# Kernel tuning notes

Hardware: AMD Instinct MI355X
Metric: run time of the kernel (lower is better)

The kernel has to match this reference:

```python
import jax, jax.numpy as jnp
import numpy as np

B, TIN, TOUT = 128, 512, 64
IN_F, OUT_F, H = 64, 32, 1024
DEC_IN = IN_F + OUT_F  # decoder GRU input size


def setup_inputs() -> dict:
    key = jax.random.key(0)
    ks = jax.random.split(key, 24)
    s = 1.0 / np.sqrt(H)
    u = lambda k, shp: jax.random.uniform(k, shp, jnp.float32, -s, s)
    return {
        "enc_input": jax.random.normal(ks[0], (B, TIN, IN_F), jnp.float32),
        "dec_input": jax.random.normal(ks[1], (B, TOUT, IN_F), jnp.float32),
        # encoder GRU, layer 0 (input IN_F) and layer 1 (input H); gates stacked [r,z,n]
        "enc_Wih0": u(ks[2], (3 * H, IN_F)), "enc_Whh0": u(ks[3], (3 * H, H)),
        "enc_bih0": u(ks[4], (3 * H,)), "enc_bhh0": u(ks[5], (3 * H,)),
        "enc_Wih1": u(ks[6], (3 * H, H)), "enc_Whh1": u(ks[7], (3 * H, H)),
        "enc_bih1": u(ks[8], (3 * H,)), "enc_bhh1": u(ks[9], (3 * H,)),
        # decoder GRU, layer 0 (input DEC_IN) and layer 1 (input H)
        "dec_Wih0": u(ks[10], (3 * H, DEC_IN)), "dec_Whh0": u(ks[11], (3 * H, H)),
        "dec_bih0": u(ks[12], (3 * H,)), "dec_bhh0": u(ks[13], (3 * H,)),
        "dec_Wih1": u(ks[14], (3 * H, H)), "dec_Whh1": u(ks[15], (3 * H, H)),
        "dec_bih1": u(ks[16], (3 * H,)), "dec_bhh1": u(ks[17], (3 * H,)),
        # output MLP: Linear(H,H)+ReLU, then Linear(H,OUT_F, bias=False)
        "out1_W": u(ks[18], (H, H)), "out1_b": u(ks[19], (H,)),
        "out2_W": u(ks[20], (OUT_F, H)),
    }


def _gru_cell(x, h, Wih, Whh, bih, bhh):
    """Single GRU step, PyTorch gate convention. x:(B,in) h:(B,H) -> (B,H)."""
    gi = x @ Wih.T + bih
    gh = h @ Whh.T + bhh
    ir, iz, inn = jnp.split(gi, 3, axis=-1)
    hr, hz, hn = jnp.split(gh, 3, axis=-1)
    r = jax.nn.sigmoid(ir + hr)
    z = jax.nn.sigmoid(iz + hz)
    n = jnp.tanh(inn + r * hn)
    return (1.0 - z) * n + z * h


def _gru_layer(x, h0, Wih, Whh, bih, bhh):
    """Full-sequence GRU layer. x:(B,T,in) -> (ys:(B,T,H), hT:(B,H))."""
    xp = jnp.einsum('bti,gi->btg', x, Wih) + bih  # precompute input projections
    def step(h, g):
        gh = h @ Whh.T + bhh
        ir, iz, inn = jnp.split(g, 3, axis=-1)
        hr, hz, hn = jnp.split(gh, 3, axis=-1)
        r = jax.nn.sigmoid(ir + hr)
        z = jax.nn.sigmoid(iz + hz)
        n = jnp.tanh(inn + r * hn)
        hnew = (1.0 - z) * n + z * h
        return hnew, hnew
    hT, ys = jax.lax.scan(step, h0, jnp.swapaxes(xp, 0, 1))
    return jnp.swapaxes(ys, 0, 1), hT


def _forward(enc_input, dec_input,
             enc_Wih0, enc_Whh0, enc_bih0, enc_bhh0,
             enc_Wih1, enc_Whh1, enc_bih1, enc_bhh1,
             dec_Wih0, dec_Whh0, dec_bih0, dec_bhh0,
             dec_Wih1, dec_Whh1, dec_bih1, dec_bhh1,
             out1_W, out1_b, out2_W):
    b = enc_input.shape[0]
    zeros = jnp.zeros((b, H), enc_input.dtype)
    # encoder: 2-layer GRU from zero state
    y0, eh0 = _gru_layer(enc_input, zeros, enc_Wih0, enc_Whh0, enc_bih0, enc_bhh0)
    _, eh1 = _gru_layer(y0, zeros, enc_Wih1, enc_Whh1, enc_bih1, enc_bhh1)
    y_prev0 = enc_input[:, -1, :OUT_F]
    def dec_step(carry, x_t):
        y_prev, h0, h1 = carry
        x = jnp.concatenate([y_prev, x_t], axis=-1)  # (B, OUT_F+IN_F)
        h0n = _gru_cell(x, h0, dec_Wih0, dec_Whh0, dec_bih0, dec_bhh0)
        h1n = _gru_cell(h0n, h1, dec_Wih1, dec_Whh1, dec_bih1, dec_bhh1)
        out = jax.nn.relu(h1n @ out1_W.T + out1_b) @ out2_W.T  # dropout=identity (eval)
        return (out, h0n, h1n), out
    _, ys = jax.lax.scan(dec_step, (y_prev0, eh0, eh1), jnp.swapaxes(dec_input, 0, 1))
    return jnp.swapaxes(ys, 0, 1)  # (B, TOUT, OUT_F)


def reference(enc_input, dec_input,
              enc_Wih0, enc_Whh0, enc_bih0, enc_bhh0,
              enc_Wih1, enc_Whh1, enc_bih1, enc_bhh1,
              dec_Wih0, dec_Whh0, dec_bih0, dec_bhh0,
              dec_Wih1, dec_Whh1, dec_bih1, dec_bhh1,
              out1_W, out1_b, out2_W):
    return _forward(enc_input, dec_input,
                    enc_Wih0, enc_Whh0, enc_bih0, enc_bhh0,
                    enc_Wih1, enc_Whh1, enc_bih1, enc_bhh1,
                    dec_Wih0, dec_Whh0, dec_bih0, dec_bhh0,
                    dec_Wih1, dec_Whh1, dec_bih1, dec_bhh1,
                    out1_W, out1_b, out2_W)
```

## Files before the change

### kernel.cpp

```cpp
#include <hip/hip_runtime.h>

typedef unsigned short u16;
typedef unsigned long long u64;
typedef __attribute__((ext_vector_type(8))) short bf16x8;
typedef __attribute__((ext_vector_type(4))) float f32x4;

#define Bsz   128
#define TIN   512
#define TOUT  64
#define INF   64
#define OUTF  32
#define Hdim  1024
#define H3    3072

#define K0    1088
#define K1    2048
#define KD0   1120
#define KD1   2048
#define KH    1024

#define SX0  (Bsz * K0)
#define SX1  (Bsz * K1)
#define SXD0 (Bsz * KD0)
#define SXD1 (Bsz * KD1)
#define SH   (Bsz * Hdim)

#define BAR_ROOT 512
#define BAR_GEN  528
#define BAR_WORDS 544

__device__ __forceinline__ u16 f2bf(float f) {
    union { float f; unsigned u; } c; c.f = f;
    unsigned u = c.u;
    unsigned r = (u + 0x7fffu + ((u >> 16) & 1u)) >> 16;
    return (u16)r;
}

__device__ __forceinline__ f32x4 mfma16(bf16x8 a, bf16x8 b, f32x4 c) {
    return __builtin_amdgcn_mfma_f32_16x16x32_bf16(a, b, c, 0, 0, 0);
}

__device__ __forceinline__ void tile_map32(int wg, int& htile, int& bq) {
    const int xcd = wg & 7, idx = wg >> 3;
    htile = ((idx & 3) << 3) + xcd;
    bq = idx >> 2;
}

__device__ __forceinline__ u64 ald64(const void* p) {
    return __hip_atomic_load((const u64*)p, __ATOMIC_RELAXED, __HIP_MEMORY_SCOPE_AGENT);
}
__device__ __forceinline__ void ast64(void* p, u64 v) {
    __hip_atomic_store((u64*)p, v, __ATOMIC_RELAXED, __HIP_MEMORY_SCOPE_AGENT);
}
__device__ __forceinline__ float aldf(const float* p) {
    return __hip_atomic_load(p, __ATOMIC_RELAXED, __HIP_MEMORY_SCOPE_AGENT);
}
__device__ __forceinline__ void astf(float* p, float v) {
    __hip_atomic_store(p, v, __ATOMIC_RELAXED, __HIP_MEMORY_SCOPE_AGENT);
}
__device__ __forceinline__ u16 aldu16(const u16* p) {
    return __hip_atomic_load(p, __ATOMIC_RELAXED, __HIP_MEMORY_SCOPE_AGENT);
}
__device__ __forceinline__ void astu16(u16* p, u16 v) {
    __hip_atomic_store(p, v, __ATOMIC_RELAXED, __HIP_MEMORY_SCOPE_AGENT);
}
__device__ __forceinline__ bf16x8 ldx(const u16* p) {
    union { u64 q[2]; bf16x8 v; } u;
    u.q[0] = ald64(p);
    u.q[1] = ald64(p + 4);
    return u.v;
}

__device__ __forceinline__ void gridbar(unsigned* bar, unsigned target) {
    __syncthreads();
    if (threadIdx.x == 0) {
        asm volatile("s_waitcnt vmcnt(0) lgkmcnt(0)" ::: "memory");
        unsigned leaf = (blockIdx.x >> 3) << 4;
        unsigned a = __hip_atomic_fetch_add(&bar[leaf], 1u,
                        __ATOMIC_RELAXED, __HIP_MEMORY_SCOPE_AGENT);
        if (((a + 1u) & 7u) == 0u) {
            unsigned r = __hip_atomic_fetch_add(&bar[BAR_ROOT], 1u,
                            __ATOMIC_RELAXED, __HIP_MEMORY_SCOPE_AGENT);
            if (((r + 1u) & 31u) == 0u)
                __hip_atomic_fetch_add(&bar[BAR_GEN], 1u,
                        __ATOMIC_RELAXED, __HIP_MEMORY_SCOPE_AGENT);
        }
        while (__hip_atomic_load(&bar[BAR_GEN],
                    __ATOMIC_RELAXED, __HIP_MEMORY_SCOPE_AGENT) < target)
            __builtin_amdgcn_s_sleep(2);
        asm volatile("" ::: "memory");
    }
    __syncthreads();
}

template <int K>
__device__ __forceinline__ void stage_x(const u16* __restrict__ Xsrc, u16* __restrict__ xl) {
    const int tid = threadIdx.x;
    const int r = tid >> 4, tj = tid & 15;
    const u16* srow = Xsrc + (size_t)r * K;
    const unsigned base = (unsigned)(r * K * 2);
    const unsigned swz = (unsigned)((r & 7) << 4);
    constexpr int U = K / 4;
    for (int k0 = tj; k0 < U; k0 += 128) {
        u64 tmp[8];
#pragma unroll
        for (int i = 0; i < 8; ++i) {
            int k4 = k0 + i * 16;
            if (k4 < U) tmp[i] = ald64(srow + k4 * 4);
        }
#pragma unroll
        for (int i = 0; i < 8; ++i) {
            int k4 = k0 + i * 16;
            if (k4 < U) *(u64*)((char*)xl + ((base + (unsigned)k4 * 8u) ^ swz)) = tmp[i];
        }
    }
}

template <int KB0, int KB1, int SPLIT, int K>
__device__ __forceinline__ void gru_wave_lds(
        const u16* __restrict__ W, const u16* __restrict__ xl,
        int j0w, int row,
        f32x4& accR, f32x4& accZ, f32x4& accN0, f32x4& accN1) {
    const int lane = threadIdx.x & 63;
    const int l15 = lane & 15, kq = lane >> 4;
    const u16* Wr = W + (size_t)(j0w + l15) * K + kq * 8;
    const u16* Wz = Wr + (size_t)1024 * K;
    const u16* Wn = Wz + (size_t)1024 * K;
    const unsigned xbase = (unsigned)(row * K * 2 + kq * 16);
    const unsigned swz = (unsigned)((row & 7) << 4);
    accR = (f32x4){0.f, 0.f, 0.f, 0.f};
    accZ = (f32x4){0.f, 0.f, 0.f, 0.f};
    accN0 = (f32x4){0.f, 0.f, 0.f, 0.f};
    accN1 = (f32x4){0.f, 0.f, 0.f, 0.f};
    constexpr int E0 = (SPLIT < KB1) ? SPLIT : KB1;
    constexpr int S1 = (SPLIT > KB0) ? SPLIT : KB0;
#pragma unroll 8
    for (int kb = KB0; kb < E0; ++kb) {
        const int o = kb * 32;
        bf16x8 xb = *(const bf16x8*)((const char*)xl + ((xbase + (unsigned)kb * 64u) ^ swz));
        accR  = mfma16(*(const bf16x8*)(Wr + o), xb, accR);
        accZ  = mfma16(*(const bf16x8*)(Wz + o), xb, accZ);
        accN0 = mfma16(*(const bf16x8*)(Wn + o), xb, accN0);
    }
#pragma unroll 8
    for (int kb = S1; kb < KB1; ++kb) {
        const int o = kb * 32;
        bf16x8 xb = *(const bf16x8*)((const char*)xl + ((xbase + (unsigned)kb * 64u) ^ swz));
        accR  = mfma16(*(const bf16x8*)(Wr + o), xb, accR);
        accZ  = mfma16(*(const bf16x8*)(Wz + o), xb, accZ);
        accN1 = mfma16(*(const bf16x8*)(Wn + o), xb, accN1);
    }
}

template <int KBT, int SPLIT, int K>
__device__ __forceinline__ void gru_block32(
        const u16* __restrict__ W, const u16* __restrict__ X,
        const float* __restrict__ Hold, const float* __restrict__ Bias,
        int htile, int bq,
        float* __restrict__ Hnew,
        u16* __restrict__ O1, int ld1, int off1,
        u16* __restrict__ O2, int ld2, int off2,
        float* __restrict__ sred , u16* __restrict__ xl) {
    stage_x<K>(X + (size_t)bq * 32 * K, xl);
    __syncthreads();

    const int tid = threadIdx.x, lane = tid & 63, w = tid >> 6;
    const int hf = w & 1, bf = (w >> 1) & 1, grp = w >> 2, bg = w & 3;
    const int l15 = lane & 15, kq = lane >> 4;
    const int j0w = htile * 32 + hf * 16;
    const int rowl = bf * 16 + l15;
    constexpr int MID = KBT / 2;

    f32x4 aR, aZ, aN0, aN1;
    if (grp == 0) gru_wave_lds<0, MID, SPLIT, K>(W, xl, j0w, rowl, aR, aZ, aN0, aN1);
    else          gru_wave_lds<MID, KBT, SPLIT, K>(W, xl, j0w, rowl, aR, aZ, aN0, aN1);

    float* slot = sred + ((size_t)bg * 64 + lane) * 17;
    if (grp == 1) {
#pragma unroll
        for (int q = 0; q < 4; ++q) {
            slot[q]      = aR[q];
            slot[4 + q]  = aZ[q];
            slot[8 + q]  = aN0[q];
            slot[12 + q] = aN1[q];
        }
    }
    __syncthreads();
    if (grp == 0) {
        const int nb = bq * 32 + bf * 16 + l15;
        float hv4[4];
#pragma unroll
        for (int q = 0; q < 4; ++q) {
            const int j = j0w + kq * 4 + q;
            float R  = aR[q]  + slot[q];
            float Z  = aZ[q]  + slot[4 + q];
            float Nh = aN0[q] + slot[8 + q];
            float Ni = aN1[q] + slot[12 + q];
            float r = 1.f / (1.f + expf(-(R + Bias[j])));
            float z = 1.f / (1.f + expf(-(Z + Bias[1024 + j])));
            float n = tanhf(Ni + Bias[2048 + j] + r * (Nh + Bias[3072 + j]));
            float ho = aldf(&Hold[(size_t)j * Bsz + nb]);
            float hv = (1.f - z) * n + z * ho;
            astf(&Hnew[(size_t)j * Bsz + nb], hv);
            hv4[q] = hv;
        }
        union { u16 h[4]; u64 q8; } pk;
#pragma unroll
        for (int q = 0; q < 4; ++q) pk.h[q] = f2bf(hv4[q]);
        ast64(&O1[(size_t)nb * ld1 + off1 + j0w + kq * 4], pk.q8);
        if (O2) ast64(&O2[(size_t)nb * ld2 + off2 + j0w + kq * 4], pk.q8);
    }
}


__global__ void __launch_bounds__(256) pack2(
        const float* __restrict__ A, int KA,
        const float* __restrict__ Bs, int KB,
        u16* __restrict__ dst) {
    int row = blockIdx.y;
    int k = blockIdx.x * 256 + threadIdx.x;
    int K = KA + KB;
    if (k >= K) return;
    float v = (k < KA) ? A[(size_t)row * KA + k] : Bs[(size_t)row * KB + (k - KA)];
    dst[(size_t)row * K + k] = f2bf(v);
}

__global__ void __launch_bounds__(256) pack_bias(
        const float* bi0e, const float* bh0e,
        const float* bi1e, const float* bh1e,
        const float* bi0d, const float* bh0d,
        const float* bi1d, const float* bh1d,
        const float* out1b,
        float* B0, float* B1, float* BD0, float* BD1, float* HB) {
    int j = blockIdx.x * blockDim.x + threadIdx.x;
    if (j >= 1024) return;
    const float* bis[4] = { bi0e, bi1e, bi0d, bi1d };
    const float* bhs[4] = { bh0e, bh1e, bh0d, bh1d };
    float* ds[4] = { B0, B1, BD0, BD1 };
#pragma unroll
    for (int s = 0; s < 4; ++s) {
        ds[s][j]        = bis[s][j]        + bhs[s][j];
        ds[s][1024 + j] = bis[s][1024 + j] + bhs[s][1024 + j];
        ds[s][2048 + j] = bis[s][2048 + j];
        ds[s][3072 + j] = bhs[s][2048 + j];
    }
    HB[j] = out1b[j];
}

__global__ void __launch_bounds__(256) init_state(
        const float* __restrict__ enc_input,
        u16* __restrict__ X0, u16* __restrict__ X1,
        float* __restrict__ H0f, float* __restrict__ H1f,
        unsigned* __restrict__ bar) {
    int gtid = blockIdx.x * blockDim.x + threadIdx.x;
    int G = gridDim.x * blockDim.x;
    for (int i = gtid; i < BAR_WORDS; i += G) bar[i] = 0u;
    for (int i = gtid; i < Bsz * Hdim; i += G) { int b = i >> 10, j = i & 1023; X0[(size_t)b * K0 + j] = 0; }
    for (int i = gtid; i < Bsz * INF; i += G) { int b = i >> 6, f = i & 63;
        X0[(size_t)b * K0 + 1024 + f] = f2bf(enc_input[(size_t)b * (TIN * INF) + f]); }
    for (int i = gtid; i < Bsz * Hdim; i += G) { int b = i >> 10, j = i & 1023;
        X1[(size_t)SX1 + (size_t)b * K1 + j] = 0; }
    for (int i = gtid; i < Bsz * Hdim; i += G) { H0f[i] = 0.f; H1f[SH + i] = 0.f; }
}

struct KParams {
    const float* enc_input;
    const float* dec_input;
    const u16 *W0, *W1, *WD0, *WD1, *WH1, *WH2;
    const float *B0, *B1, *BD0, *BD1, *HB;
    u16 *X0, *X1, *XD0, *XD1, *Hhead, *Abuf;
    float *H0f, *H1f;
    float* out;
    unsigned* bar;
};


__device__ __forceinline__ void enc_round_body(const KParams& p, int r,
                                               float* sred, u16* xl) {
    const int wg = blockIdx.x;
    const int pr = r & 1, pw = pr ^ 1;
    if (wg < 128) {
        if (r < 512) {
            int htile, bq; tile_map32(wg, htile, bq);
            gru_block32<34, 32, K0>(p.W0, p.X0 + pr * SX0, p.H0f + pr * SH, p.B0,
                                    htile, bq,
                                    p.H0f + pw * SH,
                                    p.X0 + pw * SX0, K0, 0,
                                    p.X1 + pw * SX1, K1, 1024, sred, xl);
            if (r + 1 < 512 && threadIdx.x < 16) {
                int b = wg, f4 = threadIdx.x * 4;
                const float* src = p.enc_input + ((size_t)b * TIN + (r + 1)) * INF + f4;
                union { u16 h[4]; u64 q8; } pk;
#pragma unroll
                for (int i = 0; i < 4; ++i) pk.h[i] = f2bf(src[i]);
                ast64(&p.X0[(size_t)pw * SX0 + (size_t)b * K0 + 1024 + f4], pk.q8);
            }
        }
    } else {
        if (r >= 1) {
            int htile, bq; tile_map32(wg - 128, htile, bq);
            gru_block32<64, 32, K1>(p.W1, p.X1 + pr * SX1, p.H1f + pr * SH, p.B1,
                                    htile, bq,
                                    p.H1f + pw * SH,
                                    p.X1 + pw * SX1, K1, 0,
                                    (u16*)nullptr, 0, 0, sred, xl);
        }
    }
}

__device__ __forceinline__ void transition_body(const KParams& p) {
    int gtid = blockIdx.x * blockDim.x + threadIdx.x;
    const int G = 256 * 512;
    for (int i = gtid; i < SH; i += G)
        astf(&p.H1f[i], aldf(&p.H1f[SH + i]));
    for (int i = gtid; i < Bsz * Hdim; i += G) {
        int b = i >> 10, j = i & 1023;
        astu16(&p.XD0[(size_t)b * KD0 + j], aldu16(&p.X0[(size_t)b * K0 + j]));
    }
    for (int i = gtid; i < Bsz * OUTF; i += G) {
        int b = i >> 5, f = i & 31;
        astu16(&p.XD0[(size_t)b * KD0 + 1024 + f],
               f2bf(p.enc_input[((size_t)b * TIN + (TIN - 1)) * INF + f]));
    }
    for (int i = gtid; i < Bsz * INF; i += G) {
        int b = i >> 6, f = i & 63;
        astu16(&p.XD0[(size_t)b * KD0 + 1056 + f],
               f2bf(p.dec_input[(size_t)b * (TOUT * INF) + f]));
    }
    for (int i = gtid; i < Bsz * Hdim; i += G) {
        int b = i >> 10, j = i & 1023;
        astu16(&p.XD1[(size_t)b * KD1 + j],
               aldu16(&p.X1[(size_t)SX1 + (size_t)b * K1 + j]));
    }
}

__device__ __forceinline__ void dec_A_body(const KParams& p, int t, float* sred, u16* xl) {
    const int wg = blockIdx.x;
    const int pt = t & 1, pn = pt ^ 1;
    int htile, bq; tile_map32(wg, htile, bq);
    gru_block32<35, 32, KD0>(p.WD0, p.XD0 + pt * SXD0, p.H0f + pt * SH, p.BD0,
                             htile, bq,
                             p.H0f + pn * SH,
                             p.XD0 + pn * SXD0, KD0, 0,
                             p.XD1 + pt * SXD1, KD1, 1024, sred, xl);
}

__device__ __forceinline__ void dec_B_body(const KParams& p, int t, float* sred, u16* xl) {
    const int wg = blockIdx.x;
    const int pt = t & 1, pn = pt ^ 1;
    int htile, bq; tile_map32(wg, htile, bq);
    gru_block32<64, 32, KD1>(p.WD1, p.XD1 + pt * SXD1, p.H1f + pt * SH, p.BD1,
                             htile, bq,
                             p.H1f + pn * SH,
                             p.XD1 + pn * SXD1, KD1, 0,
                             p.Hhead, KH, 0, sred, xl);
}

__device__ __forceinline__ void dec_C_body(const KParams& p, int t, float* sred, u16* xl) {
    const int wg = blockIdx.x;
    const int pn = (t & 1) ^ 1;
    int htile, bq; tile_map32(wg, htile, bq);
    stage_x<KH>(p.Hhead + (size_t)bq * 32 * KH, xl);
    __syncthreads();

    const int tid = threadIdx.x, lane = tid & 63, w = tid >> 6;
    const int hf = w & 1, bf = (w >> 1) & 1, grp = w >> 2, bg = w & 3;
    const int l15 = lane & 15, kq = lane >> 4;
    const int j0w = htile * 32 + hf * 16;
    const int rowl = bf * 16 + l15;

    const u16* Wr = p.WH1 + (size_t)(j0w + l15) * KH + kq * 8;
    const unsigned xbase = (unsigned)(rowl * KH * 2 + kq * 16);
    const unsigned swz = (unsigned)((rowl & 7) << 4);
    f32x4 acc = {0.f, 0.f, 0.f, 0.f};
    const int kb0 = grp * 16, kb1 = kb0 + 16;
#pragma unroll 8
    for (int kb = kb0; kb < kb1; ++kb) {
        bf16x8 xb = *(const bf16x8*)((const char*)xl + ((xbase + (unsigned)kb * 64u) ^ swz));
        acc = mfma16(*(const bf16x8*)(Wr + kb * 32), xb, acc);
    }
    float* slot = sred + ((size_t)bg * 64 + lane) * 17;
    if (grp == 1) {
#pragma unroll
        for (int q = 0; q < 4; ++q) slot[q] = acc[q];
    }
    __syncthreads();
    if (grp == 0) {
        const int nb = bq * 32 + bf * 16 + l15;
        union { u16 h[4]; u64 q8; } pk;
#pragma unroll
        for (int q = 0; q < 4; ++q) {
            const int j = j0w + kq * 4 + q;
            float v = acc[q] + slot[q] + p.HB[j];
            pk.h[q] = f2bf(v > 0.f ? v : 0.f);
        }
        ast64(&p.Abuf[(size_t)nb * KH + j0w + kq * 4], pk.q8);
    }
    if (t + 1 < TOUT && tid < 16) {
        int b = wg, f4 = tid * 4;
        const float* src = p.dec_input + ((size_t)b * TOUT + (t + 1)) * INF + f4;
        union { u16 h[4]; u64 q8; } pk2;
#pragma unroll
        for (int i = 0; i < 4; ++i) pk2.h[i] = f2bf(src[i]);
        ast64(&p.XD0[(size_t)pn * SXD0 + (size_t)b * KD0 + 1056 + f4], pk2.q8);
    }
}

__device__ __forceinline__ void dec_D_body(const KParams& p, int t, float* sred) {
    const int wg = blockIdx.x;
    const int pn = (t & 1) ^ 1;
    const int tid = threadIdx.x, lane = tid & 63, w = tid >> 6;
    const int l15 = lane & 15, kq = lane >> 4;
    const int mt = wg & 1, nt = wg >> 1;
    if (w < 4) {
        const u16* Wr = p.WH2 + (size_t)(mt * 16 + l15) * KH + kq * 8;
        const u16* Xb = p.Abuf + (size_t)(nt * 16 + l15) * KH + kq * 8;
        f32x4 acc = {0.f, 0.f, 0.f, 0.f};
#pragma unroll 8
        for (int kb = w * 8; kb < w * 8 + 8; ++kb) {
            const int o = kb * 32;
            acc = mfma16(*(const bf16x8*)(Wr + o), ldx(Xb + o), acc);
        }
#pragma unroll
        for (int q = 0; q < 4; ++q) sred[(w * 64 + lane) * 4 + q] = acc[q];
    }
    __syncthreads();
    if (w == 0) {
        int b = nt * 16 + l15;
        union { u16 h[4]; u64 q8; } pk;
#pragma unroll
        for (int q = 0; q < 4; ++q) {
            float s = sred[(0 * 64 + lane) * 4 + q] + sred[(1 * 64 + lane) * 4 + q] +
                      sred[(2 * 64 + lane) * 4 + q] + sred[(3 * 64 + lane) * 4 + q];
            int feat = mt * 16 + kq * 4 + q;
            p.out[(size_t)b * (TOUT * OUTF) + t * OUTF + feat] = s;
            pk.h[q] = f2bf(s);
        }
        ast64(&p.XD0[(size_t)pn * SXD0 + (size_t)b * KD0 + 1024 + mt * 16 + kq * 4], pk.q8);
    }
}

__global__ void __launch_bounds__(512, 1) seq2seq_persist(KParams p) {
    __shared__ float sred[4 * 64 * 17];
    __shared__ u16 xls[32 * 2048];
    unsigned target = 0;

    for (int r = 0; r < 513; ++r) {
        enc_round_body(p, r, sred, xls);
        gridbar(p.bar, ++target);
    }

    transition_body(p);
    gridbar(p.bar, ++target);

    for (int t = 0; t < TOUT; ++t) {
        if (blockIdx.x < 128) dec_A_body(p, t, sred, xls);
        gridbar(p.bar, ++target);
        if (blockIdx.x < 128) dec_B_body(p, t, sred, xls);
        gridbar(p.bar, ++target);
        if (blockIdx.x < 128) dec_C_body(p, t, sred, xls);
        gridbar(p.bar, ++target);
        if (blockIdx.x < 16) dec_D_body(p, t, sred);
        if (t + 1 < TOUT) gridbar(p.bar, ++target);
    }
}

extern "C" void kernel_launch(void* const* d_in, const int* in_sizes, int n_in,
                              void* d_out, int out_size, void* d_ws, size_t ws_size,
                              hipStream_t stream) {
    const float* enc_input = (const float*)d_in[0];
    const float* dec_input = (const float*)d_in[1];
    const float* enc_Wih0 = (const float*)d_in[2];
    const float* enc_Whh0 = (const float*)d_in[3];
    const float* enc_bih0 = (const float*)d_in[4];
    const float* enc_bhh0 = (const float*)d_in[5];
    const float* enc_Wih1 = (const float*)d_in[6];
    const float* enc_Whh1 = (const float*)d_in[7];
    const float* enc_bih1 = (const float*)d_in[8];
    const float* enc_bhh1 = (const float*)d_in[9];
    const float* dec_Wih0 = (const float*)d_in[10];
    const float* dec_Whh0 = (const float*)d_in[11];
    const float* dec_bih0 = (const float*)d_in[12];
    const float* dec_bhh0 = (const float*)d_in[13];
    const float* dec_Wih1 = (const float*)d_in[14];
    const float* dec_Whh1 = (const float*)d_in[15];
    const float* dec_bih1 = (const float*)d_in[16];
    const float* dec_bhh1 = (const float*)d_in[17];
    const float* out1_W = (const float*)d_in[18];
    const float* out1_b = (const float*)d_in[19];
    const float* out2_W = (const float*)d_in[20];

    char* ws = (char*)d_ws;
    size_t off = 0;
    auto alloc = [&](size_t bytes) { size_t o = off; off = (off + bytes + 255) & ~(size_t)255; return o; };

    u16* W0 = (u16*)(ws + alloc((size_t)H3 * K0 * 2));
    u16* W1 = (u16*)(ws + alloc((size_t)H3 * K1 * 2));
    u16* WD0 = (u16*)(ws + alloc((size_t)H3 * KD0 * 2));
    u16* WD1 = (u16*)(ws + alloc((size_t)H3 * KD1 * 2));
    u16* WH1 = (u16*)(ws + alloc((size_t)Hdim * KH * 2));
    u16* WH2 = (u16*)(ws + alloc((size_t)OUTF * KH * 2));
    float* B0 = (float*)(ws + alloc(4096 * 4));
    float* B1 = (float*)(ws + alloc(4096 * 4));
    float* BD0 = (float*)(ws + alloc(4096 * 4));
    float* BD1 = (float*)(ws + alloc(4096 * 4));
    float* HB = (float*)(ws + alloc(1024 * 4));
    u16* X0 = (u16*)(ws + alloc((size_t)2 * Bsz * K0 * 2));
    u16* X1 = (u16*)(ws + alloc((size_t)2 * Bsz * K1 * 2));
    u16* XD0 = (u16*)(ws + alloc((size_t)2 * Bsz * KD0 * 2));
    u16* XD1 = (u16*)(ws + alloc((size_t)2 * Bsz * KD1 * 2));
    float* H0f = (float*)(ws + alloc((size_t)2 * Bsz * Hdim * 4));
    float* H1f = (float*)(ws + alloc((size_t)2 * Bsz * Hdim * 4));
    u16* Hhead = (u16*)(ws + alloc((size_t)Bsz * KH * 2));
    u16* Abuf = (u16*)(ws + alloc((size_t)Bsz * KH * 2));
    unsigned* bar = (unsigned*)(ws + alloc(BAR_WORDS * 4));

    pack2<<<dim3((K0 + 255) / 256, H3), 256, 0, stream>>>(enc_Whh0, 1024, enc_Wih0, 64, W0);
    pack2<<<dim3((K1 + 255) / 256, H3), 256, 0, stream>>>(enc_Whh1, 1024, enc_Wih1, 1024, W1);
    pack2<<<dim3((KD0 + 255) / 256, H3), 256, 0, stream>>>(dec_Whh0, 1024, dec_Wih0, 96, WD0);
    pack2<<<dim3((KD1 + 255) / 256, H3), 256, 0, stream>>>(dec_Whh1, 1024, dec_Wih1, 1024, WD1);
    pack2<<<dim3((KH + 255) / 256, Hdim), 256, 0, stream>>>(out1_W, 1024, nullptr, 0, WH1);
    pack2<<<dim3((KH + 255) / 256, OUTF), 256, 0, stream>>>(out2_W, 1024, nullptr, 0, WH2);
    pack_bias<<<4, 256, 0, stream>>>(enc_bih0, enc_bhh0, enc_bih1, enc_bhh1,
                                     dec_bih0, dec_bhh0, dec_bih1, dec_bhh1,
                                     out1_b, B0, B1, BD0, BD1, HB);
    init_state<<<256, 256, 0, stream>>>(enc_input, X0, X1, H0f, H1f, bar);

    KParams kp;
    kp.enc_input = enc_input; kp.dec_input = dec_input;
    kp.W0 = W0; kp.W1 = W1; kp.WD0 = WD0; kp.WD1 = WD1; kp.WH1 = WH1; kp.WH2 = WH2;
    kp.B0 = B0; kp.B1 = B1; kp.BD0 = BD0; kp.BD1 = BD1; kp.HB = HB;
    kp.X0 = X0; kp.X1 = X1; kp.XD0 = XD0; kp.XD1 = XD1; kp.Hhead = Hhead; kp.Abuf = Abuf;
    kp.H0f = H0f; kp.H1f = H1f;
    kp.out = (float*)d_out;
    kp.bar = bar;

    seq2seq_persist<<<256, 512, 0, stream>>>(kp);
}
```

Before: 23.49 ms.

## Replace global grid barriers with per-batch-group producer/consumer barriers

Splits the persistent kernel's synchronisation so encoder layer 0 and layer 1 blocks, and decoder stages, sync only within 32-block batch groups using per-group generation counters. Layer 1 waits on layer 0's generation and layer 0 waits on layer 1 to bound the double-buffer lag. This replaces grid-wide barriers with finer-grained group barriers and lets the two layers run decoupled. Also widens LDS staging loads to 16-byte nontemporal loads. The risk is correctness of the buffer-reuse ordering across the independent groups.

```diff
diff --git a/kernel.cpp b/kernel.cpp
--- a/kernel.cpp
+++ b/kernel.cpp
@@ -27,7 +27,8 @@
 
 #define BAR_ROOT 512
 #define BAR_GEN  528
-#define BAR_WORDS 544
+#define GRP_BASE 1024
+#define BAR_WORDS 2048
 
 __device__ __forceinline__ u16 f2bf(float f) {
     union { float f; unsigned u; } c; c.f = f;
@@ -69,6 +70,37 @@
     u.q[0] = ald64(p);
     u.q[1] = ald64(p + 4);
     return u.v;
+}
+
+__device__ __forceinline__ void ldg16_nt(const u16* p, bf16x8& v) {
+    asm volatile("global_load_dwordx4 %0, %1, off sc0 sc1 nt"
+                 : "=&v"(v) : "v"(p));
+}
+
+template <unsigned NB>
+__device__ __forceinline__ void groupbar(unsigned* arr, unsigned* gen, unsigned target) {
+    __syncthreads();
+    if (threadIdx.x == 0) {
+        asm volatile("s_waitcnt vmcnt(0) lgkmcnt(0)" ::: "memory");
+        unsigned a = __hip_atomic_fetch_add(arr, 1u,
+                        __ATOMIC_RELAXED, __HIP_MEMORY_SCOPE_AGENT);
+        if (((a + 1u) & (NB - 1u)) == 0u)
+            __hip_atomic_fetch_add(gen, 1u,
+                        __ATOMIC_RELAXED, __HIP_MEMORY_SCOPE_AGENT);
+        while (__hip_atomic_load(gen, __ATOMIC_RELAXED, __HIP_MEMORY_SCOPE_AGENT) < target)
+            __builtin_amdgcn_s_sleep(2);
+        asm volatile("" ::: "memory");
+    }
+    __syncthreads();
+}
+
+__device__ __forceinline__ void waitgen(unsigned* gen, unsigned target) {
+    if (threadIdx.x == 0) {
+        while (__hip_atomic_load(gen, __ATOMIC_RELAXED, __HIP_MEMORY_SCOPE_AGENT) < target)
+            __builtin_amdgcn_s_sleep(2);
+        asm volatile("" ::: "memory");
+    }
+    __syncthreads();
 }
 
 __device__ __forceinline__ void gridbar(unsigned* bar, unsigned target) {
@@ -93,6 +125,60 @@
     __syncthreads();
 }
 
+__device__ __forceinline__ unsigned* grp_arr(unsigned* bar, int g) { return bar + GRP_BASE + g * 32; }
+__device__ __forceinline__ unsigned* grp_gen(unsigned* bar, int g) { return bar + GRP_BASE + g * 32 + 16; }
+
+
+__global__ void __launch_bounds__(256) pack2(
+        const float* __restrict__ A, int KA,
+        const float* __restrict__ Bs, int KB,
+        u16* __restrict__ dst) {
+    int row = blockIdx.y;
+    int k = blockIdx.x * 256 + threadIdx.x;
+    int K = KA + KB;
+    if (k >= K) return;
+    float v = (k < KA) ? A[(size_t)row * KA + k] : Bs[(size_t)row * KB + (k - KA)];
+    dst[(size_t)row * K + k] = f2bf(v);
+}
+
+__global__ void __launch_bounds__(256) pack_bias(
+        const float* bi0e, const float* bh0e,
+        const float* bi1e, const float* bh1e,
+        const float* bi0d, const float* bh0d,
+        const float* bi1d, const float* bh1d,
+        const float* out1b,
+        float* B0, float* B1, float* BD0, float* BD1, float* HB) {
+    int j = blockIdx.x * blockDim.x + threadIdx.x;
+    if (j >= 1024) return;
+    const float* bis[4] = { bi0e, bi1e, bi0d, bi1d };
+    const float* bhs[4] = { bh0e, bh1e, bh0d, bh1d };
+    float* ds[4] = { B0, B1, BD0, BD1 };
+#pragma unroll
+    for (int s = 0; s < 4; ++s) {
+        ds[s][j]        = bis[s][j]        + bhs[s][j];
+        ds[s][1024 + j] = bis[s][1024 + j] + bhs[s][1024 + j];
+        ds[s][2048 + j] = bis[s][2048 + j];
+        ds[s][3072 + j] = bhs[s][2048 + j];
+    }
+    HB[j] = out1b[j];
+}
+
+__global__ void __launch_bounds__(256) init_state(
+        const float* __restrict__ enc_input,
+        u16* __restrict__ X0, u16* __restrict__ X1,
+        float* __restrict__ H0f, float* __restrict__ H1f,
+        unsigned* __restrict__ bar) {
+    int gtid = blockIdx.x * blockDim.x + threadIdx.x;
+    int G = gridDim.x * blockDim.x;
+    for (int i = gtid; i < BAR_WORDS; i += G) bar[i] = 0u;
+    for (int i = gtid; i < Bsz * Hdim; i += G) { int b = i >> 10, j = i & 1023; X0[(size_t)b * K0 + j] = 0; }
+    for (int i = gtid; i < Bsz * INF; i += G) { int b = i >> 6, f = i & 63;
+        X0[(size_t)b * K0 + 1024 + f] = f2bf(enc_input[(size_t)b * (TIN * INF) + f]); }
+    for (int i = gtid; i < Bsz * Hdim; i += G) { int b = i >> 10, j = i & 1023;
+        X1[(size_t)SX1 + (size_t)b * K1 + j] = 0; }
+    for (int i = gtid; i < Bsz * Hdim; i += G) { H0f[i] = 0.f; H1f[SH + i] = 0.f; }
+}
+
 template <int K>
 __device__ __forceinline__ void stage_x(const u16* __restrict__ Xsrc, u16* __restrict__ xl) {
     const int tid = threadIdx.x;
@@ -100,18 +186,21 @@
     const u16* srow = Xsrc + (size_t)r * K;
     const unsigned base = (unsigned)(r * K * 2);
     const unsigned swz = (unsigned)((r & 7) << 4);
-    constexpr int U = K / 4;
+    constexpr int U = K / 8;
     for (int k0 = tj; k0 < U; k0 += 128) {
-        u64 tmp[8];
+        bf16x8 t[8];
 #pragma unroll
         for (int i = 0; i < 8; ++i) {
-            int k4 = k0 + i * 16;
-            if (k4 < U) tmp[i] = ald64(srow + k4 * 4);
-        }
+            int k = k0 + i * 16;
+            if (k < U) ldg16_nt(srow + k * 8, t[i]);
+        }
+        asm volatile("s_waitcnt vmcnt(0)" ::: "memory");
+        __builtin_amdgcn_sched_barrier(0);
 #pragma unroll
         for (int i = 0; i < 8; ++i) {
-            int k4 = k0 + i * 16;
-            if (k4 < U) *(u64*)((char*)xl + ((base + (unsigned)k4 * 8u) ^ swz)) = tmp[i];
+            int k = k0 + i * 16;
+            if (k < U)
+                *(bf16x8*)((char*)xl + ((base + (unsigned)k * 16u) ^ swz)) = t[i];
         }
     }
 }
@@ -212,57 +301,6 @@
     }
 }
 
-
-__global__ void __launch_bounds__(256) pack2(
-        const float* __restrict__ A, int KA,
-        const float* __restrict__ Bs, int KB,
-        u16* __restrict__ dst) {
-    int row = blockIdx.y;
-    int k = blockIdx.x * 256 + threadIdx.x;
-    int K = KA + KB;
-    if (k >= K) return;
-    float v = (k < KA) ? A[(size_t)row * KA + k] : Bs[(size_t)row * KB + (k - KA)];
-    dst[(size_t)row * K + k] = f2bf(v);
-}
-
-__global__ void __launch_bounds__(256) pack_bias(
-        const float* bi0e, const float* bh0e,
-        const float* bi1e, const float* bh1e,
-        const float* bi0d, const float* bh0d,
-        const float* bi1d, const float* bh1d,
-        const float* out1b,
-        float* B0, float* B1, float* BD0, float* BD1, float* HB) {
-    int j = blockIdx.x * blockDim.x + threadIdx.x;
-    if (j >= 1024) return;
-    const float* bis[4] = { bi0e, bi1e, bi0d, bi1d };
-    const float* bhs[4] = { bh0e, bh1e, bh0d, bh1d };
-    float* ds[4] = { B0, B1, BD0, BD1 };
-#pragma unroll
-    for (int s = 0; s < 4; ++s) {
-        ds[s][j]        = bis[s][j]        + bhs[s][j];
-        ds[s][1024 + j] = bis[s][1024 + j] + bhs[s][1024 + j];
-        ds[s][2048 + j] = bis[s][2048 + j];
-        ds[s][3072 + j] = bhs[s][2048 + j];
-    }
-    HB[j] = out1b[j];
-}
-
-__global__ void __launch_bounds__(256) init_state(
-        const float* __restrict__ enc_input,
-        u16* __restrict__ X0, u16* __restrict__ X1,
-        float* __restrict__ H0f, float* __restrict__ H1f,
-        unsigned* __restrict__ bar) {
-    int gtid = blockIdx.x * blockDim.x + threadIdx.x;
-    int G = gridDim.x * blockDim.x;
-    for (int i = gtid; i < BAR_WORDS; i += G) bar[i] = 0u;
-    for (int i = gtid; i < Bsz * Hdim; i += G) { int b = i >> 10, j = i & 1023; X0[(size_t)b * K0 + j] = 0; }
-    for (int i = gtid; i < Bsz * INF; i += G) { int b = i >> 6, f = i & 63;
-        X0[(size_t)b * K0 + 1024 + f] = f2bf(enc_input[(size_t)b * (TIN * INF) + f]); }
-    for (int i = gtid; i < Bsz * Hdim; i += G) { int b = i >> 10, j = i & 1023;
-        X1[(size_t)SX1 + (size_t)b * K1 + j] = 0; }
-    for (int i = gtid; i < Bsz * Hdim; i += G) { H0f[i] = 0.f; H1f[SH + i] = 0.f; }
-}
-
 struct KParams {
     const float* enc_input;
     const float* dec_input;
@@ -275,37 +313,32 @@
 };
 
 
-__device__ __forceinline__ void enc_round_body(const KParams& p, int r,
-                                               float* sred, u16* xl) {
-    const int wg = blockIdx.x;
+__device__ __forceinline__ void enc_L0_round(const KParams& p, int r, int htile, int bq,
+                                             float* sred, u16* xl) {
     const int pr = r & 1, pw = pr ^ 1;
-    if (wg < 128) {
-        if (r < 512) {
-            int htile, bq; tile_map32(wg, htile, bq);
-            gru_block32<34, 32, K0>(p.W0, p.X0 + pr * SX0, p.H0f + pr * SH, p.B0,
-                                    htile, bq,
-                                    p.H0f + pw * SH,
-                                    p.X0 + pw * SX0, K0, 0,
-                                    p.X1 + pw * SX1, K1, 1024, sred, xl);
-            if (r + 1 < 512 && threadIdx.x < 16) {
-                int b = wg, f4 = threadIdx.x * 4;
-                const float* src = p.enc_input + ((size_t)b * TIN + (r + 1)) * INF + f4;
-                union { u16 h[4]; u64 q8; } pk;
-#pragma unroll
-                for (int i = 0; i < 4; ++i) pk.h[i] = f2bf(src[i]);
-                ast64(&p.X0[(size_t)pw * SX0 + (size_t)b * K0 + 1024 + f4], pk.q8);
-            }
-        }
-    } else {
-        if (r >= 1) {
-            int htile, bq; tile_map32(wg - 128, htile, bq);
-            gru_block32<64, 32, K1>(p.W1, p.X1 + pr * SX1, p.H1f + pr * SH, p.B1,
-                                    htile, bq,
-                                    p.H1f + pw * SH,
-                                    p.X1 + pw * SX1, K1, 0,
-                                    (u16*)nullptr, 0, 0, sred, xl);
-        }
-    }
+    gru_block32<34, 32, K0>(p.W0, p.X0 + pr * SX0, p.H0f + pr * SH, p.B0,
+                            htile, bq,
+                            p.H0f + pw * SH,
+                            p.X0 + pw * SX0, K0, 0,
+                            p.X1 + pw * SX1, K1, 1024, sred, xl);
+    if (r + 1 < 512 && threadIdx.x < 16) {
+        int b = bq * 32 + htile, f4 = threadIdx.x * 4;
+        const float* src = p.enc_input + ((size_t)b * TIN + (r + 1)) * INF + f4;
+        union { u16 h[4]; u64 q8; } pk;
+#pragma unroll
+        for (int i = 0; i < 4; ++i) pk.h[i] = f2bf(src[i]);
+        ast64(&p.X0[(size_t)pw * SX0 + (size_t)b * K0 + 1024 + f4], pk.q8);
+    }
+}
+
+__device__ __forceinline__ void enc_L1_step(const KParams& p, int s, int htile, int bq,
+                                            float* sred, u16* xl) {
+    const int pr = s & 1, pw = pr ^ 1;
+    gru_block32<64, 32, K1>(p.W1, p.X1 + pr * SX1, p.H1f + pr * SH, p.B1,
+                            htile, bq,
+                            p.H1f + pw * SH,
+                            p.X1 + pw * SX1, K1, 0,
+                            (u16*)nullptr, 0, 0, sred, xl);
 }
 
 __device__ __forceinline__ void transition_body(const KParams& p) {
@@ -334,10 +367,9 @@
     }
 }
 
-__device__ __forceinline__ void dec_A_body(const KParams& p, int t, float* sred, u16* xl) {
-    const int wg = blockIdx.x;
+__device__ __forceinline__ void dec_A_body(const KParams& p, int t, int htile, int bq,
+                                           float* sred, u16* xl) {
     const int pt = t & 1, pn = pt ^ 1;
-    int htile, bq; tile_map32(wg, htile, bq);
     gru_block32<35, 32, KD0>(p.WD0, p.XD0 + pt * SXD0, p.H0f + pt * SH, p.BD0,
                              htile, bq,
                              p.H0f + pn * SH,
@@ -345,10 +377,9 @@
                              p.XD1 + pt * SXD1, KD1, 1024, sred, xl);
 }
 
-__device__ __forceinline__ void dec_B_body(const KParams& p, int t, float* sred, u16* xl) {
-    const int wg = blockIdx.x;
+__device__ __forceinline__ void dec_B_body(const KParams& p, int t, int htile, int bq,
+                                           float* sred, u16* xl) {
     const int pt = t & 1, pn = pt ^ 1;
-    int htile, bq; tile_map32(wg, htile, bq);
     gru_block32<64, 32, KD1>(p.WD1, p.XD1 + pt * SXD1, p.H1f + pt * SH, p.BD1,
                              htile, bq,
                              p.H1f + pn * SH,
@@ -356,10 +387,9 @@
                              p.Hhead, KH, 0, sred, xl);
 }
 
-__device__ __forceinline__ void dec_C_body(const KParams& p, int t, float* sred, u16* xl) {
-    const int wg = blockIdx.x;
+__device__ __forceinline__ void dec_C_body(const KParams& p, int t, int htile, int bq,
+                                           float* sred, u16* xl) {
     const int pn = (t & 1) ^ 1;
-    int htile, bq; tile_map32(wg, htile, bq);
     stage_x<KH>(p.Hhead + (size_t)bq * 32 * KH, xl);
     __syncthreads();
 
@@ -397,7 +427,7 @@
         ast64(&p.Abuf[(size_t)nb * KH + j0w + kq * 4], pk.q8);
     }
     if (t + 1 < TOUT && tid < 16) {
-        int b = wg, f4 = tid * 4;
+        int b = bq * 32 + htile, f4 = tid * 4;
         const float* src = p.dec_input + ((size_t)b * TOUT + (t + 1)) * INF + f4;
         union { u16 h[4]; u64 q8; } pk2;
 #pragma unroll
@@ -406,15 +436,16 @@
     }
 }
 
-__device__ __forceinline__ void dec_D_body(const KParams& p, int t, float* sred) {
-    const int wg = blockIdx.x;
+__device__ __forceinline__ void dec_D_body(const KParams& p, int t, int htile, int bq,
+                                           float* sred) {
     const int pn = (t & 1) ^ 1;
     const int tid = threadIdx.x, lane = tid & 63, w = tid >> 6;
     const int l15 = lane & 15, kq = lane >> 4;
-    const int mt = wg & 1, nt = wg >> 1;
+    const int mt = htile & 1, ntl = htile >> 1;
+    const int brow = bq * 32 + ntl * 16;
     if (w < 4) {
         const u16* Wr = p.WH2 + (size_t)(mt * 16 + l15) * KH + kq * 8;
-        const u16* Xb = p.Abuf + (size_t)(nt * 16 + l15) * KH + kq * 8;
+        const u16* Xb = p.Abuf + (size_t)(brow + l15) * KH + kq * 8;
         f32x4 acc = {0.f, 0.f, 0.f, 0.f};
 #pragma unroll 8
         for (int kb = w * 8; kb < w * 8 + 8; ++kb) {
@@ -426,7 +457,7 @@
     }
     __syncthreads();
     if (w == 0) {
-        int b = nt * 16 + l15;
+        int b = brow + l15;
         union { u16 h[4]; u64 q8; } pk;
 #pragma unroll
         for (int q = 0; q < 4; ++q) {
@@ -443,25 +474,54 @@
 __global__ void __launch_bounds__(512, 1) seq2seq_persist(KParams p) {
     __shared__ float sred[4 * 64 * 17];
     __shared__ u16 xls[32 * 2048];
-    unsigned target = 0;
-
-    for (int r = 0; r < 513; ++r) {
-        enc_round_body(p, r, sred, xls);
-        gridbar(p.bar, ++target);
-    }
-
+    unsigned* bar = p.bar;
+    const int wg = blockIdx.x;
+
+    if (wg < 128) {
+        int htile, bq; tile_map32(wg, htile, bq);
+        unsigned* arrL0 = grp_arr(bar, bq);
+        unsigned* genL0 = grp_gen(bar, bq);
+        unsigned* genL1 = grp_gen(bar, 4 + bq);
+        for (int r = 0; r < 512; ++r) {
+            if (r >= 2) waitgen(genL1, (unsigned)(r - 1));
+            enc_L0_round(p, r, htile, bq, sred, xls);
+            groupbar<32>(arrL0, genL0, (unsigned)(r + 1));
+        }
+    } else {
+        int htile, bq; tile_map32(wg - 128, htile, bq);
+        unsigned* arrL1 = grp_arr(bar, 4 + bq);
+        unsigned* genL1 = grp_gen(bar, 4 + bq);
+        unsigned* genL0 = grp_gen(bar, bq);
+        for (int s = 1; s <= 512; ++s) {
+            waitgen(genL0, (unsigned)s);
+            enc_L1_step(p, s, htile, bq, sred, xls);
+            groupbar<32>(arrL1, genL1, (unsigned)s);
+        }
+    }
+
+    gridbar(bar, 1);
     transition_body(p);
-    gridbar(p.bar, ++target);
-
-    for (int t = 0; t < TOUT; ++t) {
-        if (blockIdx.x < 128) dec_A_body(p, t, sred, xls);
-        gridbar(p.bar, ++target);
-        if (blockIdx.x < 128) dec_B_body(p, t, sred, xls);
-        gridbar(p.bar, ++target);
-        if (blockIdx.x < 128) dec_C_body(p, t, sred, xls);
-        gridbar(p.bar, ++target);
-        if (blockIdx.x < 16) dec_D_body(p, t, sred);
-        if (t + 1 < TOUT) gridbar(p.bar, ++target);
+    gridbar(bar, 2);
+
+    if (wg < 128) {
+        int htile, bq; tile_map32(wg, htile, bq);
+        unsigned* arrA = grp_arr(bar, 8 + bq);  unsigned* genA = grp_gen(bar, 8 + bq);
+        unsigned* arrB = grp_arr(bar, 12 + bq); unsigned* genB = grp_gen(bar, 12 + bq);
+        unsigned* arrC = grp_arr(bar, 16 + bq); unsigned* genC = grp_gen(bar, 16 + bq);
+        unsigned* arrD = grp_arr(bar, 20 + bq); unsigned* genD = grp_gen(bar, 20 + bq);
+        for (int t = 0; t < TOUT; ++t) {
+            if (t >= 1) waitgen(genD, (unsigned)t);
+            dec_A_body(p, t, htile, bq, sred, xls);
+            groupbar<32>(arrA, genA, (unsigned)(t + 1));
+            dec_B_body(p, t, htile, bq, sred, xls);
+            groupbar<32>(arrB, genB, (unsigned)(t + 1));
+            dec_C_body(p, t, htile, bq, sred, xls);
+            groupbar<32>(arrC, genC, (unsigned)(t + 1));
+            if (htile < 4) {
+                dec_D_body(p, t, htile, bq, sred);
+                groupbar<4>(arrD, genD, (unsigned)(t + 1));
+            }
+        }
     }
 }
 
```

After: 21.76 ms. 1.08x faster.
